# Optimization experiments

Hardware: AMD Instinct MI355X
Metric: run time of the kernel (lower is better)

## Reference

```python
import jax, jax.numpy as jnp
import numpy as np

SIGMA = 1.0


def _pairwise_max(q, fact_emb):
    # q: [B, N, D], fact_emb: [F, D]  (D = 3E)
    # Gaussian RBF kernel k(x,y) = exp(-||x-y||^2 / (2*sigma^2)), then max over F.
    q2 = jnp.sum(q * q, axis=-1, keepdims=True)            # [B, N, 1]
    f2 = jnp.sum(fact_emb * fact_emb, axis=-1)             # [F]
    qf = jnp.einsum('bnd,fd->bnf', q, fact_emb)            # [B, N, F]
    d2 = jnp.maximum(q2 + f2[None, None, :] - 2.0 * qf, 0.0)
    k = jnp.exp(-d2 / (2.0 * SIGMA ** 2))                  # [B, N, F]
    return jnp.max(k, axis=2)                              # [B, N]


def setup_inputs() -> dict:
    key = jax.random.key(0)
    ks = jax.random.split(key, 7)
    B, N, F, E = 8, 4000, 4000, 100
    return {
        'rel': jax.random.normal(ks[0], (B, E), jnp.float32),
        'arg1': jax.random.normal(ks[1], (B, E), jnp.float32),
        'arg2': jax.random.normal(ks[2], (B, E), jnp.float32),
        'fact_rel': jax.random.normal(ks[3], (F, E), jnp.float32),
        'fact_arg1': jax.random.normal(ks[4], (F, E), jnp.float32),
        'fact_arg2': jax.random.normal(ks[5], (F, E), jnp.float32),
        'entity_embeddings': jax.random.normal(ks[6], (N, E), jnp.float32),
    }


def reference(rel, arg1, arg2, fact_rel, fact_arg1, fact_arg2, entity_embeddings):
    B = rel.shape[0]
    N, E = entity_embeddings.shape
    fact_emb = jnp.concatenate([fact_rel, fact_arg1, fact_arg2], axis=1)  # [F, 3E]

    rel_b = jnp.broadcast_to(rel[:, None, :], (B, N, E))
    emb_b = jnp.broadcast_to(entity_embeddings[None, :, :], (B, N, E))

    # score_sp: query = [rel, arg1, entity]
    arg1_b = jnp.broadcast_to(arg1[:, None, :], (B, N, E))
    q_sp = jnp.concatenate([rel_b, arg1_b, emb_b], axis=2)  # [B, N, 3E]
    score_sp = _pairwise_max(q_sp, fact_emb)                # [B, N]

    # score_po: query = [rel, entity, arg2]
    arg2_b = jnp.broadcast_to(arg2[:, None, :], (B, N, E))
    q_po = jnp.concatenate([rel_b, emb_b, arg2_b], axis=2)  # [B, N, 3E]
    score_po = _pairwise_max(q_po, fact_emb)                # [B, N]

    return (score_sp, score_po)
```

## Files before the change

kernel.cpp:

```cpp
#include <hip/hip_runtime.h>
#include <math.h>

#define EDIM 100
#define KP   128
#define NF   4000
#define NN   4000
#define NB   8
#define NP   4096
#define BN   128
#define BF   64
#define NFB  (NP / BF)
#define TRS  68

typedef __attribute__((ext_vector_type(8))) short short8;
typedef __attribute__((ext_vector_type(4))) float floatx4;

__device__ __align__(16) unsigned short g_A [NP * KP];
__device__ __align__(16) unsigned short g_B1[NP * KP];
__device__ __align__(16) unsigned short g_B2[NP * KP];
__device__ __align__(16) float g_P[2 * NB * NP];
__device__ float g_e2[NN];
__device__ float g_part[2 * NB * NFB * NP];

__device__ __forceinline__ unsigned short f2bf(float x) {
    union { float f; unsigned int u; } v; v.f = x;
    unsigned int r = v.u + 0x7FFFu + ((v.u >> 16) & 1u);
    return (unsigned short)(r >> 16);
}

__global__ void convert(const float* __restrict__ ent,
                        const float* __restrict__ fa1,
                        const float* __restrict__ fa2) {
    int idx = blockIdx.x * 256 + threadIdx.x;
    const float* src = (blockIdx.y == 0) ? ent : (blockIdx.y == 1) ? fa1 : fa2;
    unsigned short* dst = (blockIdx.y == 0) ? g_A : (blockIdx.y == 1) ? g_B1 : g_B2;
    int row = idx >> 7, k = idx & (KP - 1);
    float v = (row < NF && k < EDIM) ? src[row * EDIM + k] : 0.f;
    dst[idx] = f2bf(v);
}

__global__ void precompute_P(const float* __restrict__ rel,
                             const float* __restrict__ arg1,
                             const float* __restrict__ arg2,
                             const float* __restrict__ frel,
                             const float* __restrict__ fa1,
                             const float* __restrict__ fa2) {
    const int t = threadIdx.x;
    const int fl = t & 15;
    const int kq = t >> 4;
    const int f = blockIdx.x * 16 + fl;
    const int b = blockIdx.y;
    const int fr = (f < NF) ? f : (NF - 1);

    float nf = 0.f, dr = 0.f, d1 = 0.f, d2 = 0.f, qr = 0.f, q1 = 0.f, q2 = 0.f;
    for (int i = 0; i < 25; i++) {
        int k = kq * 25 + i;
        float vr = frel[fr * EDIM + k];
        float v1 = fa1[fr * EDIM + k];
        float v2 = fa2[fr * EDIM + k];
        float rb = rel[b * EDIM + k];
        float a1 = arg1[b * EDIM + k];
        float a2 = arg2[b * EDIM + k];
        nf += vr * vr + v1 * v1 + v2 * v2;
        dr = fmaf(rb, vr, dr);
        d1 = fmaf(a1, v1, d1);
        d2 = fmaf(a2, v2, d2);
        qr = fmaf(rb, rb, qr);
        q1 = fmaf(a1, a1, q1);
        q2 = fmaf(a2, a2, q2);
    }
    nf += __shfl_xor(nf, 16); nf += __shfl_xor(nf, 32);
    dr += __shfl_xor(dr, 16); dr += __shfl_xor(dr, 32);
    d1 += __shfl_xor(d1, 16); d1 += __shfl_xor(d1, 32);
    d2 += __shfl_xor(d2, 16); d2 += __shfl_xor(d2, 32);
    qr += __shfl_xor(qr, 16); qr += __shfl_xor(qr, 32);
    q1 += __shfl_xor(q1, 16); q1 += __shfl_xor(q1, 32);
    q2 += __shfl_xor(q2, 16); q2 += __shfl_xor(q2, 32);
    if (kq == 0) {
        float psp = nf + qr + q1 - 2.f * (dr + d1);
        float ppo = nf + qr + q2 - 2.f * (dr + d2);
        if (f >= NF) { psp = __builtin_inff(); ppo = __builtin_inff(); }
        g_P[(0 * NB + b) * NP + f] = psp;
        g_P[(1 * NB + b) * NP + f] = ppo;
    }
}

__global__ void precompute_e2(const float* __restrict__ ent) {
    int n = blockIdx.x * 256 + threadIdx.x;
    if (n >= NN) return;
    const float4* ep = (const float4*)(ent + n * EDIM);
    float s = 0.f;
    #pragma unroll
    for (int i = 0; i < EDIM / 4; i++) {
        float4 v = ep[i];
        s += v.x * v.x + v.y * v.y + v.z * v.z + v.w * v.w;
    }
    g_e2[n] = s;
}

__global__ void __launch_bounds__(256, 2) main_kernel() {
    __shared__ float4 smem4[4352];
    float4* lA4  = smem4;
    float4* lB14 = smem4 + 2048;
    float4* lB24 = smem4 + 3072;
    float*  tr   = (float*)smem4;

    const int t = threadIdx.x;
    const int n0 = blockIdx.x * BN;
    const int fblk = blockIdx.y;
    const int f0 = fblk * BF;

    const float4* gA4 = (const float4*)g_A;
    const float4* gB14 = (const float4*)g_B1;
    const float4* gB24 = (const float4*)g_B2;
    #pragma unroll
    for (int i = 0; i < 8; i++) {
        int gc = i * 256 + t;
        int row = gc >> 4, ch = gc & 15;
        lA4[row * 16 + (ch ^ (row & 15))] = gA4[n0 * 16 + gc];
    }
    #pragma unroll
    for (int i = 0; i < 4; i++) {
        int gc = i * 256 + t;
        int row = gc >> 4, ch = gc & 15;
        int sl = row * 16 + (ch ^ (row & 15));
        lB14[sl] = gB14[f0 * 16 + gc];
        lB24[sl] = gB24[f0 * 16 + gc];
    }
    __syncthreads();

    const int lane = t & 63;
    const int c = lane & 15;
    const int q = lane >> 4;
    const int w = t >> 6;
    const int w32 = w * 32;

    const short8* pA  = (const short8*)lA4;
    const short8* pB1 = (const short8*)lB14;
    const short8* pB2 = (const short8*)lB24;

    floatx4 acc[2][2][4];
    #pragma unroll
    for (int g = 0; g < 2; g++)
        #pragma unroll
        for (int mt = 0; mt < 2; mt++)
            #pragma unroll
            for (int ft = 0; ft < 4; ft++)
                acc[g][mt][ft] = (floatx4){0.f, 0.f, 0.f, 0.f};

    #pragma unroll
    for (int s = 0; s < 4; s++) {
        const int base = s * 4 + q;
        short8 a0 = pA[(w32 + c) * 16 + (base ^ c)];
        short8 a1 = pA[(w32 + 16 + c) * 16 + (base ^ c)];
        #pragma unroll
        for (int ft = 0; ft < 4; ft++) {
            int sl = (ft * 16 + c) * 16 + (base ^ c);
            short8 b1 = pB1[sl];
            short8 b2 = pB2[sl];
            acc[0][0][ft] = __builtin_amdgcn_mfma_f32_16x16x32_bf16(a0, b2, acc[0][0][ft], 0, 0, 0);
            acc[0][1][ft] = __builtin_amdgcn_mfma_f32_16x16x32_bf16(a1, b2, acc[0][1][ft], 0, 0, 0);
            acc[1][0][ft] = __builtin_amdgcn_mfma_f32_16x16x32_bf16(a0, b1, acc[1][0][ft], 0, 0, 0);
            acc[1][1][ft] = __builtin_amdgcn_mfma_f32_16x16x32_bf16(a1, b1, acc[1][1][ft], 0, 0, 0);
        }
    }

    __syncthreads();

    #pragma unroll
    for (int g = 0; g < 2; g++)
        #pragma unroll
        for (int mt = 0; mt < 2; mt++)
            #pragma unroll
            for (int ft = 0; ft < 4; ft++)
                #pragma unroll
                for (int r = 0; r < 4; r++)
                    tr[(g * BN + w32 + mt * 16 + q * 4 + r) * TRS + ft * 16 + c] =
                        acc[g][mt][ft][r];
    __syncthreads();

    const int g2 = t >> 7;
    const int row = t & 127;
    const float4* trg = (const float4*)(tr + (g2 * BN + row) * TRS);
    float4 G4[16];
    #pragma unroll
    for (int ch = 0; ch < 16; ch++) G4[ch] = trg[ch];

    #pragma unroll
    for (int b = 0; b < NB; b++) {
        const float4* Pp = (const float4*)(g_P + (g2 * NB + b) * NP + f0);
        float4 m4 = {__builtin_inff(), __builtin_inff(), __builtin_inff(), __builtin_inff()};
        #pragma unroll
        for (int ch = 0; ch < 16; ch++) {
            float4 p = Pp[ch];
            m4.x = fminf(m4.x, fmaf(-2.f, G4[ch].x, p.x));
            m4.y = fminf(m4.y, fmaf(-2.f, G4[ch].y, p.y));
            m4.z = fminf(m4.z, fmaf(-2.f, G4[ch].z, p.z));
            m4.w = fminf(m4.w, fmaf(-2.f, G4[ch].w, p.w));
        }
        float m = fminf(fminf(m4.x, m4.y), fminf(m4.z, m4.w));
        g_part[((g2 * NB + b) * NFB + fblk) * NP + n0 + row] = m;
    }
}

__global__ void finalize(float* __restrict__ out) {
    int idx = blockIdx.x * 256 + threadIdx.x;
    if (idx >= 2 * NB * NN) return;
    int sb = idx / NN;
    int n = idx % NN;
    float m = __builtin_inff();
    #pragma unroll 8
    for (int j = 0; j < NFB; j++) m = fminf(m, g_part[(sb * NFB + j) * NP + n]);
    float d2 = fmaxf(m + g_e2[n], 0.f);
    out[idx] = expf(-0.5f * d2);
}

extern "C" void kernel_launch(void* const* d_in, const int* in_sizes, int n_in,
                              void* d_out, int out_size, void* d_ws, size_t ws_size,
                              hipStream_t stream) {
    const float* rel  = (const float*)d_in[0];
    const float* arg1 = (const float*)d_in[1];
    const float* arg2 = (const float*)d_in[2];
    const float* frel = (const float*)d_in[3];
    const float* fa1  = (const float*)d_in[4];
    const float* fa2  = (const float*)d_in[5];
    const float* ent  = (const float*)d_in[6];
    float* out = (float*)d_out;

    convert<<<dim3(NP * KP / 256, 3), 256, 0, stream>>>(ent, fa1, fa2);
    precompute_P<<<dim3(NP / 16, NB), 64, 0, stream>>>(rel, arg1, arg2, frel, fa1, fa2);
    precompute_e2<<<(NN + 255) / 256, 256, 0, stream>>>(ent);
    main_kernel<<<dim3(NP / BN, NFB), 256, 0, stream>>>();
    finalize<<<(2 * NB * NN + 255) / 256, 256, 0, stream>>>(out);
}
```

Before: 136.2 us.

## Merge prep kernels and loop four F-tiles per block to shrink partials

Folds the convert, e2 and P precompute kernels into a single launch, vectorises the bf16 conversion with float4 loads, and stages the fact and query rows in shared memory when computing P. The main kernel now walks four 64-wide F tiles per block and keeps a running min in registers, so only 16 partial-min slices are written instead of 64. This cuts launch overhead, partial-result traffic and the finalize reduction. In exchange the grid is four times smaller (512 blocks) and the A tile is reloaded into shared memory on every iteration, so there is less parallelism for hiding latency.

```diff
diff --git a/kernel.cpp b/kernel.cpp
--- a/kernel.cpp
+++ b/kernel.cpp
@@ -9,8 +9,13 @@
 #define NP   4096
 #define BN   128
 #define BF   64
-#define NFB  (NP / BF)
+#define NT   4
+#define FCH  16
 #define TRS  68
+
+#define CVT_BLOCKS 1536
+#define E2_BLOCKS  16
+#define P_BLOCKS   128
 
 typedef __attribute__((ext_vector_type(8))) short short8;
 typedef __attribute__((ext_vector_type(4))) float floatx4;
@@ -20,7 +25,7 @@
 __device__ __align__(16) unsigned short g_B2[NP * KP];
 __device__ __align__(16) float g_P[2 * NB * NP];
 __device__ float g_e2[NN];
-__device__ float g_part[2 * NB * NFB * NP];
+__device__ float g_part[2 * NB * FCH * NP];
 
 __device__ __forceinline__ unsigned short f2bf(float x) {
     union { float f; unsigned int u; } v; v.f = x;
@@ -28,74 +33,88 @@
     return (unsigned short)(r >> 16);
 }
 
-__global__ void convert(const float* __restrict__ ent,
-                        const float* __restrict__ fa1,
-                        const float* __restrict__ fa2) {
-    int idx = blockIdx.x * 256 + threadIdx.x;
-    const float* src = (blockIdx.y == 0) ? ent : (blockIdx.y == 1) ? fa1 : fa2;
-    unsigned short* dst = (blockIdx.y == 0) ? g_A : (blockIdx.y == 1) ? g_B1 : g_B2;
-    int row = idx >> 7, k = idx & (KP - 1);
-    float v = (row < NF && k < EDIM) ? src[row * EDIM + k] : 0.f;
-    dst[idx] = f2bf(v);
-}
-
-__global__ void precompute_P(const float* __restrict__ rel,
-                             const float* __restrict__ arg1,
-                             const float* __restrict__ arg2,
-                             const float* __restrict__ frel,
-                             const float* __restrict__ fa1,
-                             const float* __restrict__ fa2) {
+__global__ void __launch_bounds__(256) prep(const float* __restrict__ rel,
+                                            const float* __restrict__ arg1,
+                                            const float* __restrict__ arg2,
+                                            const float* __restrict__ frel,
+                                            const float* __restrict__ fa1,
+                                            const float* __restrict__ fa2,
+                                            const float* __restrict__ ent) {
+    __shared__ float lf[3][32][104];
+    __shared__ float lq[3][8][104];
+    const int bid = blockIdx.x;
     const int t = threadIdx.x;
-    const int fl = t & 15;
-    const int kq = t >> 4;
-    const int f = blockIdx.x * 16 + fl;
-    const int b = blockIdx.y;
-    const int fr = (f < NF) ? f : (NF - 1);
-
+
+    if (bid < CVT_BLOCKS) {
+        const int mat = bid >> 9;
+        const int g4 = ((bid & 511) * 256 + t);
+        const int rw = g4 >> 5;
+        const int ck = g4 & 31;
+        const float* src = (mat == 0) ? ent : (mat == 1) ? fa1 : fa2;
+        unsigned short* dst = (mat == 0) ? g_A : (mat == 1) ? g_B1 : g_B2;
+        float4 v = {0.f, 0.f, 0.f, 0.f};
+        if (rw < NF && ck < 25) v = ((const float4*)src)[rw * 25 + ck];
+        ushort4 o;
+        o.x = f2bf(v.x); o.y = f2bf(v.y); o.z = f2bf(v.z); o.w = f2bf(v.w);
+        ((ushort4*)dst)[g4] = o;
+        return;
+    }
+    if (bid < CVT_BLOCKS + E2_BLOCKS) {
+        int n = (bid - CVT_BLOCKS) * 256 + t;
+        if (n < NN) {
+            const float4* ep = (const float4*)(ent + n * EDIM);
+            float s = 0.f;
+            #pragma unroll
+            for (int i = 0; i < 25; i++) {
+                float4 v = ep[i];
+                s += v.x * v.x + v.y * v.y + v.z * v.z + v.w * v.w;
+            }
+            g_e2[n] = s;
+        }
+        return;
+    }
+    const int fb = bid - CVT_BLOCKS - E2_BLOCKS;
+    for (int i = t; i < 2400; i += 256) {
+        int mat = i / 800, rem = i % 800;
+        int rr = rem / 25, kc = rem % 25;
+        int gf = fb * 32 + rr;
+        const float* src = (mat == 0) ? frel : (mat == 1) ? fa1 : fa2;
+        float4 v = {0.f, 0.f, 0.f, 0.f};
+        if (gf < NF) v = ((const float4*)src)[gf * 25 + kc];
+        *(float4*)&lf[mat][rr][kc * 4] = v;
+    }
+    for (int i = t; i < 600; i += 256) {
+        int mat = i / 200, rem = i % 200;
+        int rr = rem / 25, kc = rem % 25;
+        const float* src = (mat == 0) ? rel : (mat == 1) ? arg1 : arg2;
+        *(float4*)&lq[mat][rr][kc * 4] = ((const float4*)src)[rr * 25 + kc];
+    }
+    __syncthreads();
+    const int fl = t >> 3, b = t & 7;
+    const int f = fb * 32 + fl;
     float nf = 0.f, dr = 0.f, d1 = 0.f, d2 = 0.f, qr = 0.f, q1 = 0.f, q2 = 0.f;
-    for (int i = 0; i < 25; i++) {
-        int k = kq * 25 + i;
-        float vr = frel[fr * EDIM + k];
-        float v1 = fa1[fr * EDIM + k];
-        float v2 = fa2[fr * EDIM + k];
-        float rb = rel[b * EDIM + k];
-        float a1 = arg1[b * EDIM + k];
-        float a2 = arg2[b * EDIM + k];
-        nf += vr * vr + v1 * v1 + v2 * v2;
-        dr = fmaf(rb, vr, dr);
-        d1 = fmaf(a1, v1, d1);
-        d2 = fmaf(a2, v2, d2);
-        qr = fmaf(rb, rb, qr);
-        q1 = fmaf(a1, a1, q1);
-        q2 = fmaf(a2, a2, q2);
-    }
-    nf += __shfl_xor(nf, 16); nf += __shfl_xor(nf, 32);
-    dr += __shfl_xor(dr, 16); dr += __shfl_xor(dr, 32);
-    d1 += __shfl_xor(d1, 16); d1 += __shfl_xor(d1, 32);
-    d2 += __shfl_xor(d2, 16); d2 += __shfl_xor(d2, 32);
-    qr += __shfl_xor(qr, 16); qr += __shfl_xor(qr, 32);
-    q1 += __shfl_xor(q1, 16); q1 += __shfl_xor(q1, 32);
-    q2 += __shfl_xor(q2, 16); q2 += __shfl_xor(q2, 32);
-    if (kq == 0) {
-        float psp = nf + qr + q1 - 2.f * (dr + d1);
-        float ppo = nf + qr + q2 - 2.f * (dr + d2);
-        if (f >= NF) { psp = __builtin_inff(); ppo = __builtin_inff(); }
-        g_P[(0 * NB + b) * NP + f] = psp;
-        g_P[(1 * NB + b) * NP + f] = ppo;
-    }
-}
-
-__global__ void precompute_e2(const float* __restrict__ ent) {
-    int n = blockIdx.x * 256 + threadIdx.x;
-    if (n >= NN) return;
-    const float4* ep = (const float4*)(ent + n * EDIM);
-    float s = 0.f;
-    #pragma unroll
-    for (int i = 0; i < EDIM / 4; i++) {
-        float4 v = ep[i];
-        s += v.x * v.x + v.y * v.y + v.z * v.z + v.w * v.w;
-    }
-    g_e2[n] = s;
+    for (int kc = 0; kc < 25; kc++) {
+        float4 vr = *(const float4*)&lf[0][fl][kc * 4];
+        float4 v1 = *(const float4*)&lf[1][fl][kc * 4];
+        float4 v2 = *(const float4*)&lf[2][fl][kc * 4];
+        float4 rb = *(const float4*)&lq[0][b][kc * 4];
+        float4 a1 = *(const float4*)&lq[1][b][kc * 4];
+        float4 a2 = *(const float4*)&lq[2][b][kc * 4];
+        nf += vr.x*vr.x + vr.y*vr.y + vr.z*vr.z + vr.w*vr.w
+            + v1.x*v1.x + v1.y*v1.y + v1.z*v1.z + v1.w*v1.w
+            + v2.x*v2.x + v2.y*v2.y + v2.z*v2.z + v2.w*v2.w;
+        dr += vr.x*rb.x + vr.y*rb.y + vr.z*rb.z + vr.w*rb.w;
+        d1 += v1.x*a1.x + v1.y*a1.y + v1.z*a1.z + v1.w*a1.w;
+        d2 += v2.x*a2.x + v2.y*a2.y + v2.z*a2.z + v2.w*a2.w;
+        qr += rb.x*rb.x + rb.y*rb.y + rb.z*rb.z + rb.w*rb.w;
+        q1 += a1.x*a1.x + a1.y*a1.y + a1.z*a1.z + a1.w*a1.w;
+        q2 += a2.x*a2.x + a2.y*a2.y + a2.z*a2.z + a2.w*a2.w;
+    }
+    float psp = nf + qr + q1 - 2.f * (dr + d1);
+    float ppo = nf + qr + q2 - 2.f * (dr + d2);
+    if (f >= NF) { psp = __builtin_inff(); ppo = __builtin_inff(); }
+    g_P[(0 * NB + b) * NP + f] = psp;
+    g_P[(1 * NB + b) * NP + f] = ppo;
 }
 
 __global__ void __launch_bounds__(256, 2) main_kernel() {
@@ -107,100 +126,108 @@
 
     const int t = threadIdx.x;
     const int n0 = blockIdx.x * BN;
-    const int fblk = blockIdx.y;
-    const int f0 = fblk * BF;
-
-    const float4* gA4 = (const float4*)g_A;
-    const float4* gB14 = (const float4*)g_B1;
-    const float4* gB24 = (const float4*)g_B2;
-    #pragma unroll
-    for (int i = 0; i < 8; i++) {
-        int gc = i * 256 + t;
-        int row = gc >> 4, ch = gc & 15;
-        lA4[row * 16 + (ch ^ (row & 15))] = gA4[n0 * 16 + gc];
-    }
-    #pragma unroll
-    for (int i = 0; i < 4; i++) {
-        int gc = i * 256 + t;
-        int row = gc >> 4, ch = gc & 15;
-        int sl = row * 16 + (ch ^ (row & 15));
-        lB14[sl] = gB14[f0 * 16 + gc];
-        lB24[sl] = gB24[f0 * 16 + gc];
-    }
-    __syncthreads();
+    const int fch = blockIdx.y;
 
     const int lane = t & 63;
     const int c = lane & 15;
     const int q = lane >> 4;
     const int w = t >> 6;
     const int w32 = w * 32;
-
-    const short8* pA  = (const short8*)lA4;
-    const short8* pB1 = (const short8*)lB14;
-    const short8* pB2 = (const short8*)lB24;
-
-    floatx4 acc[2][2][4];
-    #pragma unroll
-    for (int g = 0; g < 2; g++)
-        #pragma unroll
-        for (int mt = 0; mt < 2; mt++)
-            #pragma unroll
-            for (int ft = 0; ft < 4; ft++)
-                acc[g][mt][ft] = (floatx4){0.f, 0.f, 0.f, 0.f};
-
-    #pragma unroll
-    for (int s = 0; s < 4; s++) {
-        const int base = s * 4 + q;
-        short8 a0 = pA[(w32 + c) * 16 + (base ^ c)];
-        short8 a1 = pA[(w32 + 16 + c) * 16 + (base ^ c)];
-        #pragma unroll
-        for (int ft = 0; ft < 4; ft++) {
-            int sl = (ft * 16 + c) * 16 + (base ^ c);
-            short8 b1 = pB1[sl];
-            short8 b2 = pB2[sl];
-            acc[0][0][ft] = __builtin_amdgcn_mfma_f32_16x16x32_bf16(a0, b2, acc[0][0][ft], 0, 0, 0);
-            acc[0][1][ft] = __builtin_amdgcn_mfma_f32_16x16x32_bf16(a1, b2, acc[0][1][ft], 0, 0, 0);
-            acc[1][0][ft] = __builtin_amdgcn_mfma_f32_16x16x32_bf16(a0, b1, acc[1][0][ft], 0, 0, 0);
-            acc[1][1][ft] = __builtin_amdgcn_mfma_f32_16x16x32_bf16(a1, b1, acc[1][1][ft], 0, 0, 0);
-        }
-    }
-
-    __syncthreads();
-
-    #pragma unroll
-    for (int g = 0; g < 2; g++)
-        #pragma unroll
-        for (int mt = 0; mt < 2; mt++)
-            #pragma unroll
-            for (int ft = 0; ft < 4; ft++)
-                #pragma unroll
-                for (int r = 0; r < 4; r++)
-                    tr[(g * BN + w32 + mt * 16 + q * 4 + r) * TRS + ft * 16 + c] =
-                        acc[g][mt][ft][r];
-    __syncthreads();
-
     const int g2 = t >> 7;
     const int row = t & 127;
-    const float4* trg = (const float4*)(tr + (g2 * BN + row) * TRS);
-    float4 G4[16];
+
+    float m[NB];
     #pragma unroll
-    for (int ch = 0; ch < 16; ch++) G4[ch] = trg[ch];
+    for (int b = 0; b < NB; b++) m[b] = __builtin_inff();
+
+    const float4* gA4 = (const float4*)g_A;
+    const float4* gB14 = (const float4*)g_B1;
+    const float4* gB24 = (const float4*)g_B2;
+
+    for (int it = 0; it < NT; it++) {
+        const int f0 = (fch * NT + it) * BF;
+
+        #pragma unroll
+        for (int i = 0; i < 8; i++) {
+            int gc = i * 256 + t;
+            int rw = gc >> 4, ch = gc & 15;
+            lA4[rw * 16 + (ch ^ (rw & 15))] = gA4[n0 * 16 + gc];
+        }
+        #pragma unroll
+        for (int i = 0; i < 4; i++) {
+            int gc = i * 256 + t;
+            int rw = gc >> 4, ch = gc & 15;
+            int sl = rw * 16 + (ch ^ (rw & 15));
+            lB14[sl] = gB14[f0 * 16 + gc];
+            lB24[sl] = gB24[f0 * 16 + gc];
+        }
+        __syncthreads();
+
+        const short8* pA  = (const short8*)lA4;
+        const short8* pB1 = (const short8*)lB14;
+        const short8* pB2 = (const short8*)lB24;
+        floatx4 acc[2][2][4];
+        #pragma unroll
+        for (int g = 0; g < 2; g++)
+            #pragma unroll
+            for (int mt = 0; mt < 2; mt++)
+                #pragma unroll
+                for (int ft = 0; ft < 4; ft++)
+                    acc[g][mt][ft] = (floatx4){0.f, 0.f, 0.f, 0.f};
+        #pragma unroll
+        for (int s = 0; s < 4; s++) {
+            const int base = s * 4 + q;
+            short8 a0 = pA[(w32 + c) * 16 + (base ^ c)];
+            short8 a1 = pA[(w32 + 16 + c) * 16 + (base ^ c)];
+            #pragma unroll
+            for (int ft = 0; ft < 4; ft++) {
+                int sl = (ft * 16 + c) * 16 + (base ^ c);
+                short8 b1 = pB1[sl];
+                short8 b2 = pB2[sl];
+                acc[0][0][ft] = __builtin_amdgcn_mfma_f32_16x16x32_bf16(a0, b2, acc[0][0][ft], 0, 0, 0);
+                acc[0][1][ft] = __builtin_amdgcn_mfma_f32_16x16x32_bf16(a1, b2, acc[0][1][ft], 0, 0, 0);
+                acc[1][0][ft] = __builtin_amdgcn_mfma_f32_16x16x32_bf16(a0, b1, acc[1][0][ft], 0, 0, 0);
+                acc[1][1][ft] = __builtin_amdgcn_mfma_f32_16x16x32_bf16(a1, b1, acc[1][1][ft], 0, 0, 0);
+            }
+        }
+        __syncthreads();
+
+        #pragma unroll
+        for (int g = 0; g < 2; g++)
+            #pragma unroll
+            for (int mt = 0; mt < 2; mt++)
+                #pragma unroll
+                for (int ft = 0; ft < 4; ft++)
+                    #pragma unroll
+                    for (int r = 0; r < 4; r++)
+                        tr[(g * BN + w32 + mt * 16 + q * 4 + r) * TRS + ft * 16 + c] =
+                            acc[g][mt][ft][r];
+        __syncthreads();
+
+        const float4* trg = (const float4*)(tr + (g2 * BN + row) * TRS);
+        float4 G4[16];
+        #pragma unroll
+        for (int ch = 0; ch < 16; ch++) G4[ch] = trg[ch];
+        #pragma unroll
+        for (int b = 0; b < NB; b++) {
+            const float4* Pp = (const float4*)(g_P + (g2 * NB + b) * NP + f0);
+            float4 m4 = {__builtin_inff(), __builtin_inff(), __builtin_inff(), __builtin_inff()};
+            #pragma unroll
+            for (int ch = 0; ch < 16; ch++) {
+                float4 p = Pp[ch];
+                m4.x = fminf(m4.x, fmaf(-2.f, G4[ch].x, p.x));
+                m4.y = fminf(m4.y, fmaf(-2.f, G4[ch].y, p.y));
+                m4.z = fminf(m4.z, fmaf(-2.f, G4[ch].z, p.z));
+                m4.w = fminf(m4.w, fmaf(-2.f, G4[ch].w, p.w));
+            }
+            m[b] = fminf(m[b], fminf(fminf(m4.x, m4.y), fminf(m4.z, m4.w)));
+        }
+        __syncthreads();
+    }
 
     #pragma unroll
-    for (int b = 0; b < NB; b++) {
-        const float4* Pp = (const float4*)(g_P + (g2 * NB + b) * NP + f0);
-        float4 m4 = {__builtin_inff(), __builtin_inff(), __builtin_inff(), __builtin_inff()};
-        #pragma unroll
-        for (int ch = 0; ch < 16; ch++) {
-            float4 p = Pp[ch];
-            m4.x = fminf(m4.x, fmaf(-2.f, G4[ch].x, p.x));
-            m4.y = fminf(m4.y, fmaf(-2.f, G4[ch].y, p.y));
-            m4.z = fminf(m4.z, fmaf(-2.f, G4[ch].z, p.z));
-            m4.w = fminf(m4.w, fmaf(-2.f, G4[ch].w, p.w));
-        }
-        float m = fminf(fminf(m4.x, m4.y), fminf(m4.z, m4.w));
-        g_part[((g2 * NB + b) * NFB + fblk) * NP + n0 + row] = m;
-    }
+    for (int b = 0; b < NB; b++)
+        g_part[((g2 * NB + b) * FCH + fch) * NP + n0 + row] = m[b];
 }
 
 __global__ void finalize(float* __restrict__ out) {
@@ -209,8 +236,8 @@
     int sb = idx / NN;
     int n = idx % NN;
     float m = __builtin_inff();
-    #pragma unroll 8
-    for (int j = 0; j < NFB; j++) m = fminf(m, g_part[(sb * NFB + j) * NP + n]);
+    #pragma unroll
+    for (int j = 0; j < FCH; j++) m = fminf(m, g_part[(sb * FCH + j) * NP + n]);
     float d2 = fmaxf(m + g_e2[n], 0.f);
     out[idx] = expf(-0.5f * d2);
 }
@@ -227,9 +254,7 @@
     const float* ent  = (const float*)d_in[6];
     float* out = (float*)d_out;
 
-    convert<<<dim3(NP * KP / 256, 3), 256, 0, stream>>>(ent, fa1, fa2);
-    precompute_P<<<dim3(NP / 16, NB), 64, 0, stream>>>(rel, arg1, arg2, frel, fa1, fa2);
-    precompute_e2<<<(NN + 255) / 256, 256, 0, stream>>>(ent);
-    main_kernel<<<dim3(NP / BN, NFB), 256, 0, stream>>>();
+    prep<<<CVT_BLOCKS + E2_BLOCKS + P_BLOCKS, 256, 0, stream>>>(rel, arg1, arg2, frel, fa1, fa2, ent);
+    main_kernel<<<dim3(NP / BN, FCH), 256, 0, stream>>>();
     finalize<<<(2 * NB * NN + 255) / 256, 256, 0, stream>>>(out);
 }
```

After: 142.5 us. +4.6%, slower.
